# Optimization experiments

Measured on AMD Instinct MI355X. Metric: run time of the kernel, lower is better.

## Reference

```python
import jax, jax.numpy as jnp
import numpy as np

EMBED_DIM = 1024
NUM_HEADS = 16
HEAD_DIM = EMBED_DIM // NUM_HEADS


def setup_inputs() -> dict:
    key = jax.random.key(0)
    k1, k2, k3, k4 = jax.random.split(key, 4)
    S, B = 2048, 2
    x = jax.random.normal(k1, (S, B, EMBED_DIM), dtype=jnp.float32)
    # xavier_uniform for in_proj_weight [3E, E]
    limit_in = float(np.sqrt(6.0 / (3 * EMBED_DIM + EMBED_DIM)))
    in_proj_weight = jax.random.uniform(k2, (3 * EMBED_DIM, EMBED_DIM), minval=-limit_in, maxval=limit_in, dtype=jnp.float32)
    in_proj_bias = jnp.zeros((3 * EMBED_DIM,), dtype=jnp.float32)
    # out_proj: nn.Linear default init (kaiming-uniform-ish); use uniform of similar scale
    limit_out = float(np.sqrt(1.0 / EMBED_DIM))
    out_proj_weight = jax.random.uniform(k3, (EMBED_DIM, EMBED_DIM), minval=-limit_out, maxval=limit_out, dtype=jnp.float32)
    out_proj_bias = jnp.zeros((EMBED_DIM,), dtype=jnp.float32)
    return {
        "x": x,
        "in_proj_weight": in_proj_weight,
        "in_proj_bias": in_proj_bias,
        "out_proj_weight": out_proj_weight,
        "out_proj_bias": out_proj_bias,
    }


def reference(x, in_proj_weight, in_proj_bias, out_proj_weight, out_proj_bias):
    S, B, E = x.shape
    H, D = NUM_HEADS, HEAD_DIM
    scaling = float(D) ** -0.5
    # fused QKV projection: [S, B, 3E]
    qkv = jnp.einsum("sbe,fe->sbf", x, in_proj_weight) + in_proj_bias
    q, k, v = jnp.split(qkv, 3, axis=-1)
    q = q * scaling
    # [S, B, E] -> [B*H, S, D]
    def to_heads(t):
        return t.reshape(S, B * H, D).transpose(1, 0, 2)
    q, k, v = to_heads(q), to_heads(k), to_heads(v)
    # attention scores [B*H, S, S]
    scores = jnp.einsum("btd,bsd->bts", q, k)
    weights = jax.nn.softmax(scores, axis=-1)
    # dropout p=0.0 -> identity
    attn = jnp.einsum("bts,bsd->btd", weights, v)  # [B*H, S, D]
    attn = attn.transpose(1, 0, 2).reshape(S, B, E)
    out = jnp.einsum("sbe,fe->sbf", attn, out_proj_weight) + out_proj_bias
    return out
```

## Files before the change

kernel.cpp:

```cpp
#include <hip/hip_runtime.h>

typedef __bf16 bf16_t;
typedef __attribute__((ext_vector_type(8))) __bf16 bf16x8;
typedef __attribute__((ext_vector_type(4))) __bf16 bf16x4;
typedef __attribute__((ext_vector_type(4))) float f32x4;
typedef __attribute__((ext_vector_type(16))) float f32x16;
typedef __attribute__((ext_vector_type(2))) unsigned uint2v;

#define MFMA16(a, b, c) __builtin_amdgcn_mfma_f32_16x16x32_bf16((a), (b), (c), 0, 0, 0)
#define MFMA32(a, b, c) __builtin_amdgcn_mfma_f32_32x32x16_bf16((a), (b), (c), 0, 0, 0)
#define LOG2E 1.44269504088896f

__device__ __forceinline__ void async16(const bf16_t* g, bf16_t* l) {
    __builtin_amdgcn_global_load_lds(
        (const __attribute__((address_space(1))) unsigned int*)g,
        (__attribute__((address_space(3))) unsigned int*)l, 16, 0, 0);
}

__device__ __forceinline__ unsigned pack2(float a, float b) {
    union { bf16_t e[2]; unsigned u; } x;
    x.e[0] = (bf16_t)a; x.e[1] = (bf16_t)b;
    return x.u;
}

__device__ __forceinline__ void pl32swap(unsigned& a, unsigned& b) {
    uint2v r = __builtin_amdgcn_permlane32_swap(a, b, false, false);
    a = r[0]; b = r[1];
}

__device__ __forceinline__ void pbar() {
    asm volatile("" ::: "memory");
    __builtin_amdgcn_s_barrier();
    asm volatile("" ::: "memory");
}

__global__ __launch_bounds__(256) void conv3(
    const float* __restrict__ s0, const float* __restrict__ s1,
    const float* __restrict__ s2, bf16_t* __restrict__ dst,
    int n0, int n1)
{
    const int i = (blockIdx.x * 256 + threadIdx.x) * 8;
    const float* src;
    int off;
    if (i < n0)           { src = s0; off = 0; }
    else if (i < n0 + n1) { src = s1; off = n0; }
    else                  { src = s2; off = n0 + n1; }
    const float4 a = *reinterpret_cast<const float4*>(src + i - off);
    const float4 b = *reinterpret_cast<const float4*>(src + i - off + 4);
    bf16x8 o;
    o[0] = (bf16_t)a.x; o[1] = (bf16_t)a.y; o[2] = (bf16_t)a.z; o[3] = (bf16_t)a.w;
    o[4] = (bf16_t)b.x; o[5] = (bf16_t)b.y; o[6] = (bf16_t)b.z; o[7] = (bf16_t)b.w;
    *reinterpret_cast<bf16x8*>(dst + i) = o;
}

__global__ __launch_bounds__(512, 2) void gemm_qkv(
    const bf16_t* __restrict__ W, const bf16_t* __restrict__ X,
    const float* __restrict__ bias, bf16_t* __restrict__ qkv,
    bf16_t* __restrict__ vtp)
{
    constexpr int K = 1024;
    constexpr int NSTEP = K / 64;
    constexpr int AELEM = 192 * 64;
    constexpr int BELEM = 256 * 64;

    __shared__ bf16_t lds[2][AELEM + BELEM];

    const int tid  = threadIdx.x;
    const int lane = tid & 63;
    const int wv   = tid >> 6;
    const int wm   = wv >> 2;
    const int wn   = wv & 3;
    const int l15  = lane & 15;
    const int qd   = lane >> 4;

    const int id = blockIdx.x;
    const int x8 = id & 7, k = id >> 3;
    const int mb = ((k & 1) * 8 + x8) * 256;
    const int fb = (k >> 1) * 192;

    f32x4 acc[6][4] = {};

    auto stage = [&](int set, int k0) {
        bf16_t* Ab = lds[set];
        bf16_t* Bb = lds[set] + AELEM;
#pragma unroll
        for (int t = 0; t < 3; t++) {
            const int p = t * 512 + tid;
            const int r = p >> 3;
            const int c = (p & 7) ^ (r & 7);
            async16(W + (size_t)(fb + r) * K + k0 + c * 8,
                    Ab + (t * 512 + wv * 64) * 8);
        }
#pragma unroll
        for (int t = 0; t < 4; t++) {
            const int p = t * 512 + tid;
            const int r = p >> 3;
            const int c = (p & 7) ^ (r & 7);
            async16(X + (size_t)(mb + r) * K + k0 + c * 8,
                    Bb + (t * 512 + wv * 64) * 8);
        }
    };

    stage(0, 0);
    for (int s = 0; s < NSTEP; s++) {
        const int set = s & 1;
        __syncthreads();
        if (s + 1 < NSTEP) stage(set ^ 1, (s + 1) * 64);

        const bf16_t* Ab = lds[set];
        const bf16_t* Bb = lds[set] + AELEM;

        bf16x8 a0[3][2], a1[3][2], b0[2][2], b1[2][2];

#pragma unroll
        for (int i = 0; i < 3; i++) {
            const int r = wm * 96 + i * 16 + l15;
            a0[i][0] = *reinterpret_cast<const bf16x8*>(
                Ab + r * 64 + ((qd ^ (r & 7)) * 8));
            a0[i][1] = *reinterpret_cast<const bf16x8*>(
                Ab + r * 64 + (((4 + qd) ^ (r & 7)) * 8));
        }
#pragma unroll
        for (int j = 0; j < 2; j++) {
            const int r = wn * 64 + j * 16 + l15;
            b0[j][0] = *reinterpret_cast<const bf16x8*>(
                Bb + r * 64 + ((qd ^ (r & 7)) * 8));
            b0[j][1] = *reinterpret_cast<const bf16x8*>(
                Bb + r * 64 + (((4 + qd) ^ (r & 7)) * 8));
        }
        __builtin_amdgcn_s_setprio(1);
#pragma unroll
        for (int i = 0; i < 3; i++)
#pragma unroll
            for (int j = 0; j < 2; j++) {
                acc[i][j] = MFMA16(a0[i][0], b0[j][0], acc[i][j]);
                acc[i][j] = MFMA16(a0[i][1], b0[j][1], acc[i][j]);
            }
        __builtin_amdgcn_s_setprio(0);
        pbar();

#pragma unroll
        for (int i = 0; i < 3; i++) {
            const int r = wm * 96 + (i + 3) * 16 + l15;
            a1[i][0] = *reinterpret_cast<const bf16x8*>(
                Ab + r * 64 + ((qd ^ (r & 7)) * 8));
            a1[i][1] = *reinterpret_cast<const bf16x8*>(
                Ab + r * 64 + (((4 + qd) ^ (r & 7)) * 8));
        }
        __builtin_amdgcn_s_setprio(1);
#pragma unroll
        for (int i = 0; i < 3; i++)
#pragma unroll
            for (int j = 0; j < 2; j++) {
                acc[i + 3][j] = MFMA16(a1[i][0], b0[j][0], acc[i + 3][j]);
                acc[i + 3][j] = MFMA16(a1[i][1], b0[j][1], acc[i + 3][j]);
            }
        __builtin_amdgcn_s_setprio(0);
        pbar();

#pragma unroll
        for (int j = 0; j < 2; j++) {
            const int r = wn * 64 + (j + 2) * 16 + l15;
            b1[j][0] = *reinterpret_cast<const bf16x8*>(
                Bb + r * 64 + ((qd ^ (r & 7)) * 8));
            b1[j][1] = *reinterpret_cast<const bf16x8*>(
                Bb + r * 64 + (((4 + qd) ^ (r & 7)) * 8));
        }
        __builtin_amdgcn_s_setprio(1);
#pragma unroll
        for (int i = 0; i < 3; i++)
#pragma unroll
            for (int j = 0; j < 2; j++) {
                acc[i + 3][j + 2] = MFMA16(a1[i][0], b1[j][0], acc[i + 3][j + 2]);
                acc[i + 3][j + 2] = MFMA16(a1[i][1], b1[j][1], acc[i + 3][j + 2]);
            }
        __builtin_amdgcn_s_setprio(0);
        pbar();

        __builtin_amdgcn_s_setprio(1);
#pragma unroll
        for (int i = 0; i < 3; i++)
#pragma unroll
            for (int j = 0; j < 2; j++) {
                acc[i][j + 2] = MFMA16(a0[i][0], b1[j][0], acc[i][j + 2]);
                acc[i][j + 2] = MFMA16(a0[i][1], b1[j][1], acc[i][j + 2]);
            }
        __builtin_amdgcn_s_setprio(0);
    }

#pragma unroll
    for (int i = 0; i < 6; i++) {
        const int f0i = fb + wm * 96 + i * 16;
        const int f0  = f0i + qd * 4;
        const float scale = (f0i < 1024) ? 0.125f * LOG2E : 1.0f;
        const bool vblk = (f0i >= 2048);
        float bs[4];
#pragma unroll
        for (int r = 0; r < 4; r++) bs[r] = bias[f0 + r];
#pragma unroll
        for (int j = 0; j < 4; j++) {
            const int m = mb + wn * 64 + j * 16 + l15;
            if (vblk) {
                const int sIdx = m >> 1;
                const int b2   = (m & 1) << 4;
#pragma unroll
                for (int r = 0; r < 4; r++) {
                    const int fv = f0 + r - 2048;
                    vtp[(size_t)((b2 + (fv >> 6)) * 64 + (fv & 63)) * 2048 + sIdx] =
                        (bf16_t)(acc[i][j][r] + bs[r]);
                }
            } else {
                bf16x4 o;
#pragma unroll
                for (int r = 0; r < 4; r++)
                    o[r] = (bf16_t)((acc[i][j][r] + bs[r]) * scale);
                *reinterpret_cast<bf16x4*>(qkv + (size_t)m * 3072 + f0) = o;
            }
        }
    }
}

template <int MT, bool F32OUT>
__global__ __launch_bounds__(256, 3) void gemm_nt_lds(
    const bf16_t* __restrict__ W, const bf16_t* __restrict__ X,
    const float* __restrict__ bias, void* __restrict__ Cv,
    int N, int K, int fpx)
{
    constexpr int NJ = MT / 32;
    __shared__ bf16_t As[2][128 * 32];
    __shared__ bf16_t Bs[2][MT * 32];

    const int lane = threadIdx.x & 63;
    const int wv   = threadIdx.x >> 6;
    const int l15  = lane & 15;
    const int qd   = lane >> 4;

    const int id = blockIdx.x;
    const int x8 = id & 7, k = id >> 3;
    const int fb = ((k % fpx) * 8 + x8) * 128;
    const int mb = (k / fpx) * MT;
    const int fw = (wv & 1) * 64;
    const int mw = (wv >> 1) * (MT / 2);

    f32x4 acc[4][NJ] = {};

    auto stage = [&](int set, int k0) {
#pragma unroll
        for (int t = 0; t < 2; t++) {
            const int p = (wv * 2 + t) * 64 + lane;
            const int r = p >> 2, cl = (p & 3) ^ (r & 3);
            async16(W + (size_t)(fb + r) * K + k0 + cl * 8,
                    &As[set][(wv * 2 + t) * 512]);
        }
#pragma unroll
        for (int t = 0; t < MT / 64; t++) {
            const int p = (wv * (MT / 64) + t) * 64 + lane;
            const int r = p >> 2, cl = (p & 3) ^ (r & 3);
            async16(X + (size_t)(mb + r) * K + k0 + cl * 8,
                    &Bs[set][(wv * (MT / 64) + t) * 512]);
        }
    };

    stage(0, 0);
    int set = 0;
    for (int k0 = 0; k0 < K; k0 += 32) {
        __syncthreads();
        if (k0 + 32 < K) stage(set ^ 1, k0 + 32);

        const int s3 = l15 & 3;
        bf16x8 a[4], bb[NJ];
#pragma unroll
        for (int i = 0; i < 4; i++)
            a[i] = *reinterpret_cast<const bf16x8*>(
                &As[set][(fw + i * 16 + l15) * 32 + ((qd ^ s3) * 8)]);
#pragma unroll
        for (int j = 0; j < NJ; j++)
            bb[j] = *reinterpret_cast<const bf16x8*>(
                &Bs[set][(mw + j * 16 + l15) * 32 + ((qd ^ s3) * 8)]);
#pragma unroll
        for (int i = 0; i < 4; i++)
#pragma unroll
            for (int j = 0; j < NJ; j++)
                acc[i][j] = MFMA16(a[i], bb[j], acc[i][j]);
        set ^= 1;
    }

#pragma unroll
    for (int i = 0; i < 4; i++) {
        const int f0 = fb + fw + i * 16 + qd * 4;
        float bs[4];
#pragma unroll
        for (int r = 0; r < 4; r++) bs[r] = bias[f0 + r];
#pragma unroll
        for (int j = 0; j < NJ; j++) {
            const int m = mb + mw + j * 16 + l15;
            if (F32OUT) {
                float4 o;
                o.x = acc[i][j][0] + bs[0];
                o.y = acc[i][j][1] + bs[1];
                o.z = acc[i][j][2] + bs[2];
                o.w = acc[i][j][3] + bs[3];
                *reinterpret_cast<float4*>((float*)Cv + (size_t)m * N + f0) = o;
            } else {
                bf16x4 o;
#pragma unroll
                for (int r = 0; r < 4; r++)
                    o[r] = (bf16_t)(acc[i][j][r] + bs[r]);
                *reinterpret_cast<bf16x4*>((bf16_t*)Cv + (size_t)m * N + f0) = o;
            }
        }
    }
}

__global__ __launch_bounds__(256, 2) void flash_attn(
    const bf16_t* __restrict__ qkv, const bf16_t* __restrict__ vT,
    bf16_t* __restrict__ attn, int S, int B)
{
    const int E3 = 3072, E = 1024;
    const int bh = blockIdx.x, b = bh >> 4, h = bh & 15;
    const int tid = threadIdx.x, lane = tid & 63, wv = tid >> 6;
    const int qw = wv & 1;
    const int pr = wv >> 1;
    const int l31 = lane & 31, half = lane >> 5;

    __shared__ bf16_t Kt[2][2][64 * 64];
    __shared__ bf16_t Vt[2][2][64 * 64];
    __shared__ float  lsh[2][64];

    const int q0 = blockIdx.y * 128 + qw * 64;

    bf16x8 qf[2][4];
#pragma unroll
    for (int qt = 0; qt < 2; qt++) {
        const bf16_t* qp = qkv + (size_t)((q0 + qt * 32 + l31) * B + b) * E3 + h * 64;
#pragma unroll
        for (int ks = 0; ks < 4; ks++)
            qf[qt][ks] = *reinterpret_cast<const bf16x8*>(qp + ks * 16 + half * 8);
    }

    f32x16 oacc[2][2] = {};
    float lrun[2] = {0.0f, 0.0f};

    auto stage = [&](int set, int kv) {
#pragma unroll
        for (int t = 0; t < 4; t++) {
            const int p = (qw * 4 + t) * 64 + lane;
            const int r = p >> 3, cl = (p & 7) ^ (r & 7);
            async16(qkv + (size_t)((kv + r) * B + b) * E3 + E + h * 64 + cl * 8,
                    &Kt[pr][set][(qw * 4 + t) * 512]);
            async16(vT + (size_t)(bh * 64 + r) * 2048 + kv + cl * 8,
                    &Vt[pr][set][(qw * 4 + t) * 512]);
        }
    };

    const int kvbase = pr * (S / 2);
    const int NIT = S / 128;

    stage(0, kvbase);
    int set = 0;
    for (int it = 0; it < NIT; it++) {
        __syncthreads();
        if (it + 1 < NIT) stage(set ^ 1, kvbase + (it + 1) * 64);

        const bf16_t* K_ = Kt[pr][set];
        const bf16_t* V_ = Vt[pr][set];

        union PF { unsigned u[4]; bf16x8 v; };
        PF pf[2][4];
#pragma unroll
        for (int nt = 0; nt < 2; nt++) {
            const int r = nt * 32 + l31;
            const int r7 = r & 7;
            bf16x8 kf[4];
#pragma unroll
            for (int ks = 0; ks < 4; ks++)
                kf[ks] = *reinterpret_cast<const bf16x8*>(
                    K_ + r * 64 + (((ks * 2 + half) ^ r7) * 8));
#pragma unroll
            for (int qt = 0; qt < 2; qt++) {
                f32x16 st = {};
                __builtin_amdgcn_s_setprio(1);
#pragma unroll
                for (int ks = 0; ks < 4; ks++)
                    st = MFMA32(kf[ks], qf[qt][ks], st);
                __builtin_amdgcn_s_setprio(0);
                float ls = 0.0f;
                unsigned q8[8];
#pragma unroll
                for (int g = 0; g < 4; g++) {
                    const float p0 = __builtin_amdgcn_exp2f(st[4 * g]);
                    const float p1 = __builtin_amdgcn_exp2f(st[4 * g + 1]);
                    const float p2 = __builtin_amdgcn_exp2f(st[4 * g + 2]);
                    const float p3 = __builtin_amdgcn_exp2f(st[4 * g + 3]);
                    ls += (p0 + p1) + (p2 + p3);
                    q8[2 * g]     = pack2(p0, p1);
                    q8[2 * g + 1] = pack2(p2, p3);
                }
                lrun[qt] += ls;
                pl32swap(q8[0], q8[2]); pl32swap(q8[1], q8[3]);
                pl32swap(q8[4], q8[6]); pl32swap(q8[5], q8[7]);
                pf[qt][nt * 2 + 0].u[0] = q8[0]; pf[qt][nt * 2 + 0].u[1] = q8[1];
                pf[qt][nt * 2 + 0].u[2] = q8[2]; pf[qt][nt * 2 + 0].u[3] = q8[3];
                pf[qt][nt * 2 + 1].u[0] = q8[4]; pf[qt][nt * 2 + 1].u[1] = q8[5];
                pf[qt][nt * 2 + 1].u[2] = q8[6]; pf[qt][nt * 2 + 1].u[3] = q8[7];
            }
        }
        __builtin_amdgcn_s_setprio(1);
#pragma unroll
        for (int kn = 0; kn < 4; kn++)
#pragma unroll
            for (int dt = 0; dt < 2; dt++) {
                const int d = dt * 32 + l31;
                bf16x8 vf = *reinterpret_cast<const bf16x8*>(
                    V_ + d * 64 + (((kn * 2 + half) ^ (d & 7)) * 8));
                oacc[0][dt] = MFMA32(vf, pf[0][kn].v, oacc[0][dt]);
                oacc[1][dt] = MFMA32(vf, pf[1][kn].v, oacc[1][dt]);
            }
        __builtin_amdgcn_s_setprio(0);
        set ^= 1;
    }

    __syncthreads();
    float lr[2];
#pragma unroll
    for (int qt = 0; qt < 2; qt++) lr[qt] = lrun[qt] + __shfl_xor(lrun[qt], 32);

    float* fo = reinterpret_cast<float*>(&Kt[0][0][0]) + qw * 4096;

    if (pr == 1) {
#pragma unroll
        for (int qt = 0; qt < 2; qt++) {
            const int ql = qt * 32 + l31;
            lsh[qw][ql] = lr[qt];
#pragma unroll
            for (int dt = 0; dt < 2; dt++)
#pragma unroll
                for (int g = 0; g < 4; g++)
#pragma unroll
                    for (int r = 0; r < 4; r++) {
                        const int d = dt * 32 + g * 8 + half * 4 + r;
                        fo[d * 64 + ql] = oacc[qt][dt][4 * g + r];
                    }
        }
    }
    __syncthreads();
    if (pr == 0) {
#pragma unroll
        for (int qt = 0; qt < 2; qt++) {
            const int ql = qt * 32 + l31;
            const float inv = 1.0f / (lr[qt] + lsh[qw][ql]);
            const int qrow = q0 + qt * 32 + l31;
#pragma unroll
            for (int dt = 0; dt < 2; dt++)
#pragma unroll
                for (int g = 0; g < 4; g++) {
                    bf16x4 o;
#pragma unroll
                    for (int r = 0; r < 4; r++) {
                        const int d = dt * 32 + g * 8 + half * 4 + r;
                        o[r] = (bf16_t)((oacc[qt][dt][4 * g + r] + fo[d * 64 + ql]) * inv);
                    }
                    *reinterpret_cast<bf16x4*>(attn + (size_t)(qrow * B + b) * E +
                                               h * 64 + dt * 32 + g * 8 + half * 4) = o;
                }
        }
    }
}

extern "C" void kernel_launch(void* const* d_in, const int* in_sizes, int n_in,
                              void* d_out, int out_size, void* d_ws, size_t ws_size,
                              hipStream_t stream) {
    const float* x  = (const float*)d_in[0];
    const float* wi = (const float*)d_in[1];
    const float* bi = (const float*)d_in[2];
    const float* wo = (const float*)d_in[3];
    const float* bo = (const float*)d_in[4];
    float* out = (float*)d_out;

    const int S = 2048, B = 2, E = 1024;
    const int M = S * B;

    bf16_t* xb   = (bf16_t*)d_ws;
    bf16_t* wib  = xb  + (size_t)M * E;
    bf16_t* wob  = wib + (size_t)3 * E * E;
    bf16_t* qkv  = wob + (size_t)E * E;
    bf16_t* vT   = qkv + (size_t)M * 3 * E;
    bf16_t* attn = xb;

    const int n0 = M * E, n1 = 3 * E * E, n2 = E * E;
    conv3<<<(n0 + n1 + n2) / 8 / 256, 256, 0, stream>>>(x, wi, wo, xb, n0, n1);

    gemm_qkv<<<256, 512, 0, stream>>>(wib, xb, bi, qkv, vT);

    flash_attn<<<dim3(B * 16, S / 128), 256, 0, stream>>>(qkv, vT, attn, S, B);

    gemm_nt_lds<64, true><<<(E / 128) * (M / 64), 256, 0, stream>>>(
        wob, attn, bo, out, E, E, 1);
}
```

Measured before the change: 183.6 us.

## Software-pipeline flash attention so PV of previous tile overlaps QK of current

Restructures the flash attention main loop so the P·V MFMAs for iteration it-1 are interleaved with the QK^T MFMAs and exp2 work of iteration it. P fragments are double-buffered in registers (pfA/pfB), and K and V staging are split so each is loaded one iteration apart. The goal is to hide softmax/exp latency behind matrix-core work. In exchange it raises register pressure from the second P buffer, which may hurt occupancy at launch_bounds(256,2), and it adds an epilogue PV step.

```diff
diff --git a/kernel.cpp b/kernel.cpp
--- a/kernel.cpp
+++ b/kernel.cpp
@@ -312,6 +312,66 @@
     }
 }
 
+#define FLASH_ITER(IT, PW, PR)                                               \
+  {                                                                          \
+    __syncthreads();                                                         \
+    if ((IT) + 1 < NIT) stageK(set ^ 1, kvbase + ((IT) + 1) * 64);           \
+    if ((IT) > 0)       stageV((IT) & 1, kvbase + (IT) * 64);                \
+    const bf16_t* K_ = Kt[pr][set];                                          \
+    const bf16_t* Vp = Vt[pr][((IT) & 1) ^ 1];                               \
+    const bool doPV = (IT) > 0;                                              \
+    _Pragma("unroll")                                                        \
+    for (int nt = 0; nt < 2; nt++) {                                         \
+      const int r = nt * 32 + l31;                                           \
+      const int r7 = r & 7;                                                  \
+      bf16x8 kf[4];                                                          \
+      _Pragma("unroll")                                                      \
+      for (int ks = 0; ks < 4; ks++)                                         \
+        kf[ks] = *reinterpret_cast<const bf16x8*>(                           \
+            K_ + r * 64 + (((ks * 2 + half) ^ r7) * 8));                     \
+      _Pragma("unroll")                                                      \
+      for (int qt = 0; qt < 2; qt++) {                                       \
+        f32x16 st = {};                                                      \
+        __builtin_amdgcn_s_setprio(1);                                       \
+        _Pragma("unroll")                                                    \
+        for (int ks = 0; ks < 4; ks++)                                       \
+          st = MFMA32(kf[ks], qf[qt][ks], st);                               \
+        if (doPV) {                                                          \
+          const int kn = nt * 2 + qt;                                        \
+          _Pragma("unroll")                                                  \
+          for (int dt = 0; dt < 2; dt++) {                                   \
+            const int d = dt * 32 + l31;                                     \
+            bf16x8 vf = *reinterpret_cast<const bf16x8*>(                    \
+                Vp + d * 64 + (((kn * 2 + half) ^ (d & 7)) * 8));            \
+            oacc[0][dt] = MFMA32(vf, PR[0][kn].v, oacc[0][dt]);              \
+            oacc[1][dt] = MFMA32(vf, PR[1][kn].v, oacc[1][dt]);              \
+          }                                                                  \
+        }                                                                    \
+        __builtin_amdgcn_s_setprio(0);                                       \
+        float ls = 0.0f;                                                     \
+        unsigned q8[8];                                                      \
+        _Pragma("unroll")                                                    \
+        for (int g = 0; g < 4; g++) {                                        \
+          const float p0 = __builtin_amdgcn_exp2f(st[4 * g]);                \
+          const float p1 = __builtin_amdgcn_exp2f(st[4 * g + 1]);            \
+          const float p2 = __builtin_amdgcn_exp2f(st[4 * g + 2]);            \
+          const float p3 = __builtin_amdgcn_exp2f(st[4 * g + 3]);            \
+          ls += (p0 + p1) + (p2 + p3);                                       \
+          q8[2 * g]     = pack2(p0, p1);                                     \
+          q8[2 * g + 1] = pack2(p2, p3);                                     \
+        }                                                                    \
+        lrun[qt] += ls;                                                      \
+        pl32swap(q8[0], q8[2]); pl32swap(q8[1], q8[3]);                      \
+        pl32swap(q8[4], q8[6]); pl32swap(q8[5], q8[7]);                      \
+        PW[qt][nt * 2 + 0].u[0] = q8[0]; PW[qt][nt * 2 + 0].u[1] = q8[1];    \
+        PW[qt][nt * 2 + 0].u[2] = q8[2]; PW[qt][nt * 2 + 0].u[3] = q8[3];    \
+        PW[qt][nt * 2 + 1].u[0] = q8[4]; PW[qt][nt * 2 + 1].u[1] = q8[5];    \
+        PW[qt][nt * 2 + 1].u[2] = q8[6]; PW[qt][nt * 2 + 1].u[3] = q8[7];    \
+      }                                                                      \
+    }                                                                        \
+    set ^= 1;                                                                \
+  }
+
 __global__ __launch_bounds__(256, 2) void flash_attn(
     const bf16_t* __restrict__ qkv, const bf16_t* __restrict__ vT,
     bf16_t* __restrict__ attn, int S, int B)
@@ -341,70 +401,42 @@
     f32x16 oacc[2][2] = {};
     float lrun[2] = {0.0f, 0.0f};
 
-    auto stage = [&](int set, int kv) {
+    auto stageK = [&](int set_, int kv) {
 #pragma unroll
         for (int t = 0; t < 4; t++) {
             const int p = (qw * 4 + t) * 64 + lane;
             const int r = p >> 3, cl = (p & 7) ^ (r & 7);
             async16(qkv + (size_t)((kv + r) * B + b) * E3 + E + h * 64 + cl * 8,
-                    &Kt[pr][set][(qw * 4 + t) * 512]);
+                    &Kt[pr][set_][(qw * 4 + t) * 512]);
+        }
+    };
+    auto stageV = [&](int vset, int kv) {
+#pragma unroll
+        for (int t = 0; t < 4; t++) {
+            const int p = (qw * 4 + t) * 64 + lane;
+            const int r = p >> 3, cl = (p & 7) ^ (r & 7);
             async16(vT + (size_t)(bh * 64 + r) * 2048 + kv + cl * 8,
-                    &Vt[pr][set][(qw * 4 + t) * 512]);
+                    &Vt[pr][vset][(qw * 4 + t) * 512]);
         }
     };
+
+    union PF { unsigned u[4]; bf16x8 v; };
+    PF pfA[2][4], pfB[2][4];
 
     const int kvbase = pr * (S / 2);
     const int NIT = S / 128;
 
-    stage(0, kvbase);
+    stageK(0, kvbase);
+    stageV(0, kvbase);
     int set = 0;
-    for (int it = 0; it < NIT; it++) {
-        __syncthreads();
-        if (it + 1 < NIT) stage(set ^ 1, kvbase + (it + 1) * 64);
-
-        const bf16_t* K_ = Kt[pr][set];
-        const bf16_t* V_ = Vt[pr][set];
-
-        union PF { unsigned u[4]; bf16x8 v; };
-        PF pf[2][4];
-#pragma unroll
-        for (int nt = 0; nt < 2; nt++) {
-            const int r = nt * 32 + l31;
-            const int r7 = r & 7;
-            bf16x8 kf[4];
-#pragma unroll
-            for (int ks = 0; ks < 4; ks++)
-                kf[ks] = *reinterpret_cast<const bf16x8*>(
-                    K_ + r * 64 + (((ks * 2 + half) ^ r7) * 8));
-#pragma unroll
-            for (int qt = 0; qt < 2; qt++) {
-                f32x16 st = {};
-                __builtin_amdgcn_s_setprio(1);
-#pragma unroll
-                for (int ks = 0; ks < 4; ks++)
-                    st = MFMA32(kf[ks], qf[qt][ks], st);
-                __builtin_amdgcn_s_setprio(0);
-                float ls = 0.0f;
-                unsigned q8[8];
-#pragma unroll
-                for (int g = 0; g < 4; g++) {
-                    const float p0 = __builtin_amdgcn_exp2f(st[4 * g]);
-                    const float p1 = __builtin_amdgcn_exp2f(st[4 * g + 1]);
-                    const float p2 = __builtin_amdgcn_exp2f(st[4 * g + 2]);
-                    const float p3 = __builtin_amdgcn_exp2f(st[4 * g + 3]);
-                    ls += (p0 + p1) + (p2 + p3);
-                    q8[2 * g]     = pack2(p0, p1);
-                    q8[2 * g + 1] = pack2(p2, p3);
-                }
-                lrun[qt] += ls;
-                pl32swap(q8[0], q8[2]); pl32swap(q8[1], q8[3]);
-                pl32swap(q8[4], q8[6]); pl32swap(q8[5], q8[7]);
-                pf[qt][nt * 2 + 0].u[0] = q8[0]; pf[qt][nt * 2 + 0].u[1] = q8[1];
-                pf[qt][nt * 2 + 0].u[2] = q8[2]; pf[qt][nt * 2 + 0].u[3] = q8[3];
-                pf[qt][nt * 2 + 1].u[0] = q8[4]; pf[qt][nt * 2 + 1].u[1] = q8[5];
-                pf[qt][nt * 2 + 1].u[2] = q8[6]; pf[qt][nt * 2 + 1].u[3] = q8[7];
-            }
-        }
+    for (int it = 0; it < NIT; it += 2) {
+        FLASH_ITER(it,     pfA, pfB)
+        FLASH_ITER(it + 1, pfB, pfA)
+    }
+
+    __syncthreads();
+    {
+        const bf16_t* Vp = Vt[pr][(NIT - 1) & 1];
         __builtin_amdgcn_s_setprio(1);
 #pragma unroll
         for (int kn = 0; kn < 4; kn++)
@@ -412,15 +444,13 @@
             for (int dt = 0; dt < 2; dt++) {
                 const int d = dt * 32 + l31;
                 bf16x8 vf = *reinterpret_cast<const bf16x8*>(
-                    V_ + d * 64 + (((kn * 2 + half) ^ (d & 7)) * 8));
-                oacc[0][dt] = MFMA32(vf, pf[0][kn].v, oacc[0][dt]);
-                oacc[1][dt] = MFMA32(vf, pf[1][kn].v, oacc[1][dt]);
+                    Vp + d * 64 + (((kn * 2 + half) ^ (d & 7)) * 8));
+                oacc[0][dt] = MFMA32(vf, pfB[0][kn].v, oacc[0][dt]);
+                oacc[1][dt] = MFMA32(vf, pfB[1][kn].v, oacc[1][dt]);
             }
         __builtin_amdgcn_s_setprio(0);
-        set ^= 1;
-    }
-
-    __syncthreads();
+    }
+
     float lr[2];
 #pragma unroll
     for (int qt = 0; qt < 2; qt++) lr[qt] = lrun[qt] + __shfl_xor(lrun[qt], 32);
```

After: 182.2 us. No clear change (-0.8%).

## Replace output projection GEMM with 512-thread 64x256 tile kernel

Applied to the files above, without the earlier changes.

The generic output-projection GEMM (128x64 tiles, K-step 32, 256 threads) is replaced by a specialized kernel with 512 threads, 64 output-feature by 256 token tiles, and K-step 64 with 8-way XOR swizzled LDS. The inner loop is split into two halves separated by a partial barrier, and MFMA issue is wrapped in s_setprio. The aim is to halve the number of barriers per K and raise operand reuse per LDS load. The cost is larger LDS use per block and a grid of 256 blocks, which may underfill the GPU's CUs.

```diff
diff --git a/kernel.cpp b/kernel.cpp
--- a/kernel.cpp
+++ b/kernel.cpp
@@ -220,94 +220,124 @@
     }
 }
 
-template <int MT, bool F32OUT>
-__global__ __launch_bounds__(256, 3) void gemm_nt_lds(
+__global__ __launch_bounds__(512, 2) void gemm_out(
     const bf16_t* __restrict__ W, const bf16_t* __restrict__ X,
-    const float* __restrict__ bias, void* __restrict__ Cv,
-    int N, int K, int fpx)
+    const float* __restrict__ bias, float* __restrict__ out)
 {
-    constexpr int NJ = MT / 32;
-    __shared__ bf16_t As[2][128 * 32];
-    __shared__ bf16_t Bs[2][MT * 32];
-
-    const int lane = threadIdx.x & 63;
-    const int wv   = threadIdx.x >> 6;
+    constexpr int K = 1024;
+    constexpr int NSTEP = K / 64;
+    constexpr int AELEM = 64 * 64;
+    constexpr int BELEM = 256 * 64;
+
+    __shared__ bf16_t lds[2][AELEM + BELEM];
+
+    const int tid  = threadIdx.x;
+    const int lane = tid & 63;
+    const int wv   = tid >> 6;
+    const int wm   = wv >> 2;
+    const int wn   = wv & 3;
     const int l15  = lane & 15;
     const int qd   = lane >> 4;
 
     const int id = blockIdx.x;
     const int x8 = id & 7, k = id >> 3;
-    const int fb = ((k % fpx) * 8 + x8) * 128;
-    const int mb = (k / fpx) * MT;
-    const int fw = (wv & 1) * 64;
-    const int mw = (wv >> 1) * (MT / 2);
-
-    f32x4 acc[4][NJ] = {};
+    const int mb = ((k & 1) * 8 + x8) * 256;
+    const int fb = (k >> 1) * 64;
+
+    f32x4 acc[2][4] = {};
 
     auto stage = [&](int set, int k0) {
-#pragma unroll
-        for (int t = 0; t < 2; t++) {
-            const int p = (wv * 2 + t) * 64 + lane;
-            const int r = p >> 2, cl = (p & 3) ^ (r & 3);
-            async16(W + (size_t)(fb + r) * K + k0 + cl * 8,
-                    &As[set][(wv * 2 + t) * 512]);
-        }
-#pragma unroll
-        for (int t = 0; t < MT / 64; t++) {
-            const int p = (wv * (MT / 64) + t) * 64 + lane;
-            const int r = p >> 2, cl = (p & 3) ^ (r & 3);
-            async16(X + (size_t)(mb + r) * K + k0 + cl * 8,
-                    &Bs[set][(wv * (MT / 64) + t) * 512]);
+        bf16_t* Ab = lds[set];
+        bf16_t* Bb = lds[set] + AELEM;
+        {
+            const int p = tid;
+            const int r = p >> 3;
+            const int c = (p & 7) ^ (r & 7);
+            async16(W + (size_t)(fb + r) * K + k0 + c * 8,
+                    Ab + (wv * 64) * 8);
+        }
+#pragma unroll
+        for (int t = 0; t < 4; t++) {
+            const int p = t * 512 + tid;
+            const int r = p >> 3;
+            const int c = (p & 7) ^ (r & 7);
+            async16(X + (size_t)(mb + r) * K + k0 + c * 8,
+                    Bb + (t * 512 + wv * 64) * 8);
         }
     };
 
     stage(0, 0);
-    int set = 0;
-    for (int k0 = 0; k0 < K; k0 += 32) {
+    for (int s = 0; s < NSTEP; s++) {
+        const int set = s & 1;
         __syncthreads();
-        if (k0 + 32 < K) stage(set ^ 1, k0 + 32);
-
-        const int s3 = l15 & 3;
-        bf16x8 a[4], bb[NJ];
-#pragma unroll
-        for (int i = 0; i < 4; i++)
-            a[i] = *reinterpret_cast<const bf16x8*>(
-                &As[set][(fw + i * 16 + l15) * 32 + ((qd ^ s3) * 8)]);
-#pragma unroll
-        for (int j = 0; j < NJ; j++)
-            bb[j] = *reinterpret_cast<const bf16x8*>(
-                &Bs[set][(mw + j * 16 + l15) * 32 + ((qd ^ s3) * 8)]);
-#pragma unroll
-        for (int i = 0; i < 4; i++)
-#pragma unroll
-            for (int j = 0; j < NJ; j++)
-                acc[i][j] = MFMA16(a[i], bb[j], acc[i][j]);
-        set ^= 1;
-    }
-
-#pragma unroll
-    for (int i = 0; i < 4; i++) {
-        const int f0 = fb + fw + i * 16 + qd * 4;
+        if (s + 1 < NSTEP) stage(set ^ 1, (s + 1) * 64);
+
+        const bf16_t* Ab = lds[set];
+        const bf16_t* Bb = lds[set] + AELEM;
+
+        bf16x8 a[2][2], b0[2][2], b1[2][2];
+
+#pragma unroll
+        for (int i = 0; i < 2; i++) {
+            const int r = wm * 32 + i * 16 + l15;
+            a[i][0] = *reinterpret_cast<const bf16x8*>(
+                Ab + r * 64 + ((qd ^ (r & 7)) * 8));
+            a[i][1] = *reinterpret_cast<const bf16x8*>(
+                Ab + r * 64 + (((4 + qd) ^ (r & 7)) * 8));
+        }
+#pragma unroll
+        for (int j = 0; j < 2; j++) {
+            const int r = wn * 64 + j * 16 + l15;
+            b0[j][0] = *reinterpret_cast<const bf16x8*>(
+                Bb + r * 64 + ((qd ^ (r & 7)) * 8));
+            b0[j][1] = *reinterpret_cast<const bf16x8*>(
+                Bb + r * 64 + (((4 + qd) ^ (r & 7)) * 8));
+        }
+        __builtin_amdgcn_s_setprio(1);
+#pragma unroll
+        for (int i = 0; i < 2; i++)
+#pragma unroll
+            for (int j = 0; j < 2; j++) {
+                acc[i][j] = MFMA16(a[i][0], b0[j][0], acc[i][j]);
+                acc[i][j] = MFMA16(a[i][1], b0[j][1], acc[i][j]);
+            }
+        __builtin_amdgcn_s_setprio(0);
+        pbar();
+
+#pragma unroll
+        for (int j = 0; j < 2; j++) {
+            const int r = wn * 64 + (j + 2) * 16 + l15;
+            b1[j][0] = *reinterpret_cast<const bf16x8*>(
+                Bb + r * 64 + ((qd ^ (r & 7)) * 8));
+            b1[j][1] = *reinterpret_cast<const bf16x8*>(
+                Bb + r * 64 + (((4 + qd) ^ (r & 7)) * 8));
+        }
+        __builtin_amdgcn_s_setprio(1);
+#pragma unroll
+        for (int i = 0; i < 2; i++)
+#pragma unroll
+            for (int j = 0; j < 2; j++) {
+                acc[i][j + 2] = MFMA16(a[i][0], b1[j][0], acc[i][j + 2]);
+                acc[i][j + 2] = MFMA16(a[i][1], b1[j][1], acc[i][j + 2]);
+            }
+        __builtin_amdgcn_s_setprio(0);
+    }
+
+#pragma unroll
+    for (int i = 0; i < 2; i++) {
+        const int f0 = fb + wm * 32 + i * 16 + qd * 4;
         float bs[4];
 #pragma unroll
         for (int r = 0; r < 4; r++) bs[r] = bias[f0 + r];
 #pragma unroll
-        for (int j = 0; j < NJ; j++) {
-            const int m = mb + mw + j * 16 + l15;
-            if (F32OUT) {
-                float4 o;
-                o.x = acc[i][j][0] + bs[0];
-                o.y = acc[i][j][1] + bs[1];
-                o.z = acc[i][j][2] + bs[2];
-                o.w = acc[i][j][3] + bs[3];
-                *reinterpret_cast<float4*>((float*)Cv + (size_t)m * N + f0) = o;
-            } else {
-                bf16x4 o;
-#pragma unroll
-                for (int r = 0; r < 4; r++)
-                    o[r] = (bf16_t)(acc[i][j][r] + bs[r]);
-                *reinterpret_cast<bf16x4*>((bf16_t*)Cv + (size_t)m * N + f0) = o;
-            }
+        for (int j = 0; j < 4; j++) {
+            const int m = mb + wn * 64 + j * 16 + l15;
+            float4 o;
+            o.x = acc[i][j][0] + bs[0];
+            o.y = acc[i][j][1] + bs[1];
+            o.z = acc[i][j][2] + bs[2];
+            o.w = acc[i][j][3] + bs[3];
+            *reinterpret_cast<float4*>(out + (size_t)m * 1024 + f0) = o;
         }
     }
 }
@@ -494,6 +524,5 @@
 
     flash_attn<<<dim3(B * 16, S / 128), 256, 0, stream>>>(qkv, vT, attn, S, B);
 
-    gemm_nt_lds<64, true><<<(E / 128) * (M / 64), 256, 0, stream>>>(
-        wob, attn, bo, out, E, E, 1);
-}
+    gemm_out<<<256, 512, 0, stream>>>(wob, attn, bo, out);
+}
```

New measurement: 177.7 us, median of 2. -3.2%, faster.
